# Optimization experiments

Hardware: AMD Instinct MI355X
Metric: run time of the kernel (lower is better)

The kernel has to match this reference:

```python
import jax, jax.numpy as jnp
import numpy as np

# dims
P = 16            # patch size
IMG = 224
D = 768           # embed dim
DEPTH = 12
DI = 1536         # d_inner = expand * D
N = 16            # d_state
DCONV = 4
DTR = 48          # dt_rank = ceil(D / 16)
GS = IMG // P     # 14
L = GS * GS       # 196
KEEP = 49         # (1 - 0.75) * 196
EPS = 1e-5


def _pos2d(embed_dim, gs):
    # replicates get_2d_sincos_pos_embed (numpy, fp32)
    def emb1(ed, pos):
        omega = np.arange(ed // 2, dtype=np.float32) / (ed / 2.0)
        omega = 1.0 / 10000 ** omega
        out = np.einsum('m,d->md', pos.reshape(-1).astype(np.float32), omega)
        return np.concatenate([np.sin(out), np.cos(out)], axis=1)
    gh = np.arange(gs, dtype=np.float32)
    grid = np.meshgrid(gh, gh)  # (w, h) per source
    return np.concatenate([emb1(embed_dim // 2, grid[0]), emb1(embed_dim // 2, grid[1])], axis=1)


def _ln(x, w, b):
    mu = x.mean(-1, keepdims=True)
    var = ((x - mu) ** 2).mean(-1, keepdims=True)
    return (x - mu) * jax.lax.rsqrt(var + EPS) * w + b


def setup_inputs() -> dict:
    key = jax.random.key(0)
    ks = jax.random.split(key, 12)
    s = 0.02
    dt = jnp.exp(jax.random.uniform(ks[7], (DEPTH, DI)) * (np.log(0.1) - np.log(0.001)) + np.log(0.001))
    return {
        'imgs': jax.random.normal(ks[0], (8, 3, IMG, IMG), jnp.float32),
        'noise': jax.random.uniform(ks[1], (8, L), jnp.float32),
        'patch_w': s * jax.random.normal(ks[2], (D, 3, P, P), jnp.float32),
        'patch_b': jnp.zeros((D,), jnp.float32),
        'pos_embed': jnp.asarray(_pos2d(D, GS), jnp.float32),            # [L, D]
        'ln_w': jnp.ones((DEPTH, D), jnp.float32),
        'ln_b': jnp.zeros((DEPTH, D), jnp.float32),
        'in_proj_w': s * jax.random.normal(ks[3], (DEPTH, 2 * DI, D), jnp.float32),
        'conv_w': 0.1 * jax.random.normal(ks[4], (DEPTH, DI, 1, DCONV), jnp.float32),
        'conv_b': jnp.zeros((DEPTH, DI), jnp.float32),
        'x_proj_w': s * jax.random.normal(ks[5], (DEPTH, DTR + 2 * N, DI), jnp.float32),
        'dt_w': s * jax.random.normal(ks[6], (DEPTH, DI, DTR), jnp.float32),
        'dt_b': jnp.log(jnp.expm1(dt)),                                   # inverse softplus
        'A_log': jnp.broadcast_to(jnp.log(jnp.arange(1, N + 1, dtype=jnp.float32)), (DEPTH, DI, N)).copy(),
        'D_skip': jnp.ones((DEPTH, DI), jnp.float32),
        'ssm_ln_w': jnp.ones((DEPTH, DI), jnp.float32),
        'ssm_ln_b': jnp.zeros((DEPTH, DI), jnp.float32),
        'out_proj_w': s * jax.random.normal(ks[8], (DEPTH, D, DI), jnp.float32),
        'final_ln_w': jnp.ones((D,), jnp.float32),
        'final_ln_b': jnp.zeros((D,), jnp.float32),
    }


def _encoder(imgs, noise, patch_w, patch_b, pos_embed, ln_w, ln_b, in_proj_w, conv_w,
             conv_b, x_proj_w, dt_w, dt_b, A_log, D_skip, ssm_ln_w, ssm_ln_b,
             out_proj_w, final_ln_w, final_ln_b):
    B = imgs.shape[0]
    # patch embed: conv stride=kernel=P -> [B, D, 14, 14] -> [B, L, D]
    x = jax.lax.conv_general_dilated(imgs, patch_w, (P, P), 'VALID',
                                     dimension_numbers=('NCHW', 'OIHW', 'NCHW'))
    x = (x + patch_b[None, :, None, None]).reshape(B, D, L).transpose(0, 2, 1)
    x = x + pos_embed[None]

    # random masking (MAE): keep KEEP tokens per sample
    ids_shuffle = jnp.argsort(noise, axis=1)
    ids_restore = jnp.argsort(ids_shuffle, axis=1)
    ids_keep = ids_shuffle[:, :KEEP]
    x = jnp.take_along_axis(x, ids_keep[:, :, None], axis=1)  # [B, KEEP, D]
    mask = jnp.ones((B, L), jnp.float32).at[:, :KEEP].set(0.0)
    mask = jnp.take_along_axis(mask, ids_restore, axis=1)

    def block_step(carry, lp):
        hs, res = carry
        lnw, lnb, ipw, cw, cb, xpw, dtw, dtb, alog, dsk, slw, slb, opw = lp
        res = res + hs                       # Add
        h = _ln(res, lnw, lnb)               # LN
        # --- Mamba mixer ---
        xz = h @ ipw.T                       # [B,K,2*DI]
        xi, z = jnp.split(xz, 2, axis=-1)
        xc = xi.transpose(0, 2, 1)           # [B,DI,K]
        xc = jnp.pad(xc, ((0, 0), (0, 0), (DCONV - 1, 0)))  # causal depthwise conv
        xc = jax.lax.conv_general_dilated(xc, cw, (1,), 'VALID',
                                          dimension_numbers=('NCH', 'OIH', 'NCH'),
                                          feature_group_count=DI)
        xc = jax.nn.silu(xc + cb[None, :, None]).transpose(0, 2, 1)  # [B,K,DI]
        xdbl = xc @ xpw.T                    # [B,K,DTR+2N]
        dtr, Bm, Cm = jnp.split(xdbl, [DTR, DTR + N], axis=-1)
        dt = jax.nn.softplus(dtr @ dtw.T + dtb)      # [B,K,DI]
        A = -jnp.exp(alog)                            # [DI,N]
        dA = jnp.exp(dt[..., None] * A)               # [B,K,DI,N]
        dBx = (dt * xc)[..., None] * Bm[:, :, None, :]
        def scan_step(hstate, inp):
            dA_t, dBx_t, C_t = inp
            hstate = dA_t * hstate + dBx_t            # [B,DI,N]
            y = jnp.einsum('bdn,bn->bd', hstate, C_t)
            return hstate, y
        h0 = jnp.zeros((xc.shape[0], DI, N), xc.dtype)
        _, ys = jax.lax.scan(scan_step, h0,
                             (dA.transpose(1, 0, 2, 3), dBx.transpose(1, 0, 2, 3), Cm.transpose(1, 0, 2)))
        y = ys.transpose(1, 0, 2) + dsk * xc          # D skip
        y = _ln(y, slw, slb)                           # norm after SSM
        y = y * jax.nn.silu(z)                         # gate
        out = y @ opw.T                                # [B,K,D]
        return (out, res), None

    res0 = jnp.zeros_like(x)
    (hs, res), _ = jax.lax.scan(block_step, (x, res0),
                                (ln_w, ln_b, in_proj_w, conv_w, conv_b, x_proj_w, dt_w,
                                 dt_b, A_log, D_skip, ssm_ln_w, ssm_ln_b, out_proj_w))
    latent = _ln(res + hs, final_ln_w, final_ln_b)
    return latent, mask, ids_restore


def reference(imgs, noise, patch_w, patch_b, pos_embed, ln_w, ln_b, in_proj_w, conv_w,
              conv_b, x_proj_w, dt_w, dt_b, A_log, D_skip, ssm_ln_w, ssm_ln_b,
              out_proj_w, final_ln_w, final_ln_b):
    return _encoder(imgs, noise, patch_w, patch_b, pos_embed, ln_w, ln_b, in_proj_w,
                    conv_w, conv_b, x_proj_w, dt_w, dt_b, A_log, D_skip, ssm_ln_w,
                    ssm_ln_b, out_proj_w, final_ln_w, final_ln_b)
```

## Files before the change

kernel.cpp:

```cpp
#include <hip/hip_runtime.h>
#include <cstdint>
#include <cstddef>

namespace {

constexpr int kD    = 768;
constexpr int kDI   = 1536;
constexpr int kN    = 16;
constexpr int kDTR  = 48;
constexpr int kL    = 196;
constexpr int kKeep = 49;
constexpr int kB    = 8;
constexpr int kTok  = kB * kKeep;
constexpr int kPatchRows = kB * kL;
constexpr float kEps = 1e-5f;

typedef __attribute__((ext_vector_type(8))) short short8;
typedef __attribute__((ext_vector_type(4))) float f32x4;

__device__ __forceinline__ short f2bf(float f) {
  unsigned u = __float_as_uint(f);
  return (short)((u + 0x7FFFu + ((u >> 16) & 1u)) >> 16);
}

__device__ __forceinline__ short8 pack8(float4 a, float4 b) {
  short8 r;
  r[0] = f2bf(a.x); r[1] = f2bf(a.y); r[2] = f2bf(a.z); r[3] = f2bf(a.w);
  r[4] = f2bf(b.x); r[5] = f2bf(b.y); r[6] = f2bf(b.z); r[7] = f2bf(b.w);
  return r;
}

__device__ __forceinline__ float silu(float x) { return x / (1.f + expf(-x)); }

__device__ __forceinline__ float block_sum256(float x, float* sbuf) {
#pragma unroll
  for (int o = 32; o > 0; o >>= 1) x += __shfl_down(x, o, 64);
  int wid = threadIdx.x >> 6;
  if ((threadIdx.x & 63) == 0) sbuf[wid] = x;
  __syncthreads();
  float r = sbuf[0] + sbuf[1] + sbuf[2] + sbuf[3];
  __syncthreads();
  return r;
}

__global__ __launch_bounds__(256) void im2col_kernel(const float* __restrict__ imgs,
                                                     float* __restrict__ A2) {
  int idx = blockIdx.x * 256 + threadIdx.x;
  if (idx >= kPatchRows * kD) return;
  int col = idx % kD;
  int row = idx / kD;
  int b = row / kL, l = row % kL;
  int gy = l / 14, gx = l % 14;
  int c   = col >> 8;
  int rem = col & 255;
  int py = rem >> 4, px = rem & 15;
  A2[idx] = imgs[((b * 3 + c) * 224 + gy * 16 + py) * 224 + gx * 16 + px];
}

template <int SPLIT, int ACT, bool KG>
__global__ __launch_bounds__(256) void gemm_mfma(const float* __restrict__ A, int lda,
                                                 const float* __restrict__ W,
                                                 const float* __restrict__ bias,
                                                 float* __restrict__ C, int ldc,
                                                 int M, int N, int K) {
  __shared__ __align__(16) short As[8][64][8];
  __shared__ __align__(16) short Bs[8][64][8];
  const int tid = threadIdx.x;
  const int bm = blockIdx.x * 64;
  const int bn = blockIdx.y * 64;
  const int kc = K / SPLIT;
  const int k0 = blockIdx.z * kc;
  const int nk = (kc + 63) / 64;
  const int sr = tid >> 2;
  const int sq = tid & 3;
  const int lane = tid & 63;
  const int wm = ((tid >> 6) >> 1) * 32;
  const int wn = ((tid >> 6) & 1) * 32;
  const bool mok = (bm + sr) < M;
  const bool nok = (bn + sr) < N;
  const float* Ap = A + (size_t)(bm + sr) * lda + k0 + sq * 16;
  const float* Wp = W + (size_t)(bn + sr) * K + k0 + sq * 16;

  f32x4 acc[2][2];
#pragma unroll
  for (int i = 0; i < 2; ++i)
#pragma unroll
    for (int j = 0; j < 2; ++j) acc[i][j] = (f32x4){0.f, 0.f, 0.f, 0.f};

  for (int kt = 0; kt < nk; ++kt) {
    const int kb = kt * 64;
    const float4 z4 = make_float4(0.f, 0.f, 0.f, 0.f);
    float4 a0 = z4, a1 = z4, a2 = z4, a3 = z4;
    float4 w0 = z4, w1 = z4, w2 = z4, w3 = z4;
    const float* ap = Ap + kb;
    const float* wp = Wp + kb;
    if (!KG) {
      if (mok) {
        a0 = *(const float4*)ap;       a1 = *(const float4*)(ap + 4);
        a2 = *(const float4*)(ap + 8); a3 = *(const float4*)(ap + 12);
      }
      if (nok) {
        w0 = *(const float4*)wp;       w1 = *(const float4*)(wp + 4);
        w2 = *(const float4*)(wp + 8); w3 = *(const float4*)(wp + 12);
      }
    } else {
      const int kq = k0 + kb + sq * 16;
      if (mok) {
        if (kq + 4  <= K) a0 = *(const float4*)ap;
        if (kq + 8  <= K) a1 = *(const float4*)(ap + 4);
        if (kq + 12 <= K) a2 = *(const float4*)(ap + 8);
        if (kq + 16 <= K) a3 = *(const float4*)(ap + 12);
      }
      if (nok) {
        if (kq + 4  <= K) w0 = *(const float4*)wp;
        if (kq + 8  <= K) w1 = *(const float4*)(wp + 4);
        if (kq + 12 <= K) w2 = *(const float4*)(wp + 8);
        if (kq + 16 <= K) w3 = *(const float4*)(wp + 12);
      }
    }
    if (kt) __syncthreads();
    *(short8*)&As[sq * 2][sr][0]     = pack8(a0, a1);
    *(short8*)&As[sq * 2 + 1][sr][0] = pack8(a2, a3);
    *(short8*)&Bs[sq * 2][sr][0]     = pack8(w0, w1);
    *(short8*)&Bs[sq * 2 + 1][sr][0] = pack8(w2, w3);
    __syncthreads();
#pragma unroll
    for (int kh = 0; kh < 2; ++kh) {
      const int kg = kh * 4 + (lane >> 4);
      short8 af0 = *(const short8*)&As[kg][wm + (lane & 15)][0];
      short8 af1 = *(const short8*)&As[kg][wm + 16 + (lane & 15)][0];
      short8 bf0 = *(const short8*)&Bs[kg][wn + (lane & 15)][0];
      short8 bf1 = *(const short8*)&Bs[kg][wn + 16 + (lane & 15)][0];
      acc[0][0] = __builtin_amdgcn_mfma_f32_16x16x32_bf16(af0, bf0, acc[0][0], 0, 0, 0);
      acc[0][1] = __builtin_amdgcn_mfma_f32_16x16x32_bf16(af0, bf1, acc[0][1], 0, 0, 0);
      acc[1][0] = __builtin_amdgcn_mfma_f32_16x16x32_bf16(af1, bf0, acc[1][0], 0, 0, 0);
      acc[1][1] = __builtin_amdgcn_mfma_f32_16x16x32_bf16(af1, bf1, acc[1][1], 0, 0, 0);
    }
  }

  const int mrow = (lane >> 4) * 4;
  const int ncol = lane & 15;
#pragma unroll
  for (int i2 = 0; i2 < 2; ++i2)
#pragma unroll
    for (int j2 = 0; j2 < 2; ++j2) {
      int n = bn + wn + j2 * 16 + ncol;
      if (n >= N) continue;
      float bv = (SPLIT == 1 && bias) ? bias[n] : 0.f;
#pragma unroll
      for (int r = 0; r < 4; ++r) {
        int m = bm + wm + i2 * 16 + mrow + r;
        if (m >= M) continue;
        float v = acc[i2][j2][r];
        if (SPLIT == 1) {
          v += bv;
          if (ACT == 1) v = (v > 20.f) ? v : log1pf(expf(v));
          C[(size_t)m * ldc + n] = v;
        } else {
          C[(size_t)blockIdx.z * ((size_t)M * N) + (size_t)m * N + n] = v;
        }
      }
    }
}

__global__ __launch_bounds__(256) void gemm_xdbl_conv(const float* __restrict__ xz,
                                                      const float* __restrict__ cw,
                                                      const float* __restrict__ cb,
                                                      const float* __restrict__ W,
                                                      float* __restrict__ Cpart) {
  __shared__ __align__(16) short As[8][64][8];
  __shared__ __align__(16) short Bs[8][64][8];
  const int tid = threadIdx.x;
  const int bm = blockIdx.x * 64;
  const int bn = blockIdx.y * 64;
  const int k0 = blockIdx.z * 64;
  const int sr = tid >> 2;
  const int sq = tid & 3;
  const int lane = tid & 63;
  const int wm = ((tid >> 6) >> 1) * 32;
  const int wn = ((tid >> 6) & 1) * 32;
  const int m = bm + sr;
  const bool mok = m < kTok;
  const bool nok = (bn + sr) < 80;
  const float4 z4 = make_float4(0.f, 0.f, 0.f, 0.f);

  float4 a[4] = {z4, z4, z4, z4};
  if (mok) {
    const int b = m / kKeep, t = m % kKeep;
    const int dbase = k0 + sq * 16;
#pragma unroll
    for (int g = 0; g < 4; ++g) {
      const int d = dbase + g * 4;
      float4 cacc = *(const float4*)&cb[d];
      float4 c0 = *(const float4*)&cw[(d + 0) * 4];
      float4 c1 = *(const float4*)&cw[(d + 1) * 4];
      float4 c2 = *(const float4*)&cw[(d + 2) * 4];
      float4 c3 = *(const float4*)&cw[(d + 3) * 4];
      const float t0[4] = {c0.x, c0.y, c0.z, c0.w};
      const float t1[4] = {c1.x, c1.y, c1.z, c1.w};
      const float t2[4] = {c2.x, c2.y, c2.z, c2.w};
      const float t3[4] = {c3.x, c3.y, c3.z, c3.w};
#pragma unroll
      for (int j = 0; j < 4; ++j) {
        int tt = t - 3 + j;
        if (tt < 0) continue;
        float4 xv = *(const float4*)&xz[(size_t)(b * kKeep + tt) * 3072 + d];
        cacc.x += xv.x * t0[j];
        cacc.y += xv.y * t1[j];
        cacc.z += xv.z * t2[j];
        cacc.w += xv.w * t3[j];
      }
      cacc.x = silu(cacc.x); cacc.y = silu(cacc.y);
      cacc.z = silu(cacc.z); cacc.w = silu(cacc.w);
      a[g] = cacc;
    }
  }
  float4 w0 = z4, w1 = z4, w2 = z4, w3 = z4;
  if (nok) {
    const float* wp = W + (size_t)(bn + sr) * kDI + k0 + sq * 16;
    w0 = *(const float4*)wp;       w1 = *(const float4*)(wp + 4);
    w2 = *(const float4*)(wp + 8); w3 = *(const float4*)(wp + 12);
  }
  *(short8*)&As[sq * 2][sr][0]     = pack8(a[0], a[1]);
  *(short8*)&As[sq * 2 + 1][sr][0] = pack8(a[2], a[3]);
  *(short8*)&Bs[sq * 2][sr][0]     = pack8(w0, w1);
  *(short8*)&Bs[sq * 2 + 1][sr][0] = pack8(w2, w3);
  __syncthreads();

  f32x4 acc[2][2];
#pragma unroll
  for (int i = 0; i < 2; ++i)
#pragma unroll
    for (int j = 0; j < 2; ++j) acc[i][j] = (f32x4){0.f, 0.f, 0.f, 0.f};
#pragma unroll
  for (int kh = 0; kh < 2; ++kh) {
    const int kg = kh * 4 + (lane >> 4);
    short8 af0 = *(const short8*)&As[kg][wm + (lane & 15)][0];
    short8 af1 = *(const short8*)&As[kg][wm + 16 + (lane & 15)][0];
    short8 bf0 = *(const short8*)&Bs[kg][wn + (lane & 15)][0];
    short8 bf1 = *(const short8*)&Bs[kg][wn + 16 + (lane & 15)][0];
    acc[0][0] = __builtin_amdgcn_mfma_f32_16x16x32_bf16(af0, bf0, acc[0][0], 0, 0, 0);
    acc[0][1] = __builtin_amdgcn_mfma_f32_16x16x32_bf16(af0, bf1, acc[0][1], 0, 0, 0);
    acc[1][0] = __builtin_amdgcn_mfma_f32_16x16x32_bf16(af1, bf0, acc[1][0], 0, 0, 0);
    acc[1][1] = __builtin_amdgcn_mfma_f32_16x16x32_bf16(af1, bf1, acc[1][1], 0, 0, 0);
  }

  const int mrow = (lane >> 4) * 4;
  const int ncol = lane & 15;
#pragma unroll
  for (int i2 = 0; i2 < 2; ++i2)
#pragma unroll
    for (int j2 = 0; j2 < 2; ++j2) {
      int n = bn + wn + j2 * 16 + ncol;
      if (n >= 80) continue;
#pragma unroll
      for (int r = 0; r < 4; ++r) {
        int mm = bm + wm + i2 * 16 + mrow + r;
        if (mm >= kTok) continue;
        Cpart[(size_t)blockIdx.z * (kTok * 80) + (size_t)mm * 80 + n] =
            acc[i2][j2][r];
      }
    }
}

__global__ __launch_bounds__(256) void reduce_kernel(const float* __restrict__ part,
                                                     float* __restrict__ out,
                                                     int total4, int Z) {
  int i = blockIdx.x * 256 + threadIdx.x;
  if (i >= total4) return;
  const float4* p = (const float4*)part;
  float4 s = p[i];
  for (int z = 1; z < Z; ++z) {
    float4 v = p[(size_t)z * total4 + i];
    s.x += v.x; s.y += v.y; s.z += v.z; s.w += v.w;
  }
  ((float4*)out)[i] = s;
}

__global__ __launch_bounds__(256) void sort_kernel(const float* __restrict__ noise,
                                                   int* __restrict__ ids_keep,
                                                   float* __restrict__ mask_out,
                                                   float* __restrict__ idsr_out) {
  __shared__ float nb[kL];
  int b = blockIdx.x;
  int t = threadIdx.x;
  if (t < kL) nb[t] = noise[b * kL + t];
  __syncthreads();
  if (t < kL) {
    float v = nb[t];
    int rank = 0;
    for (int j = 0; j < kL; ++j) {
      float u = nb[j];
      rank += (u < v || (u == v && j < t)) ? 1 : 0;
    }
    if (rank < kKeep) ids_keep[b * kKeep + rank] = t;
    idsr_out[b * kL + t] = (float)rank;
    mask_out[b * kL + t] = (rank < kKeep) ? 0.f : 1.f;
  }
}

__global__ __launch_bounds__(256) void gather_kernel(const float* __restrict__ x0,
                                                     const int* __restrict__ ids_keep,
                                                     const float* __restrict__ pos,
                                                     float* __restrict__ hs) {
  int m = blockIdx.x;
  int b = m / kKeep, k = m % kKeep;
  int l = ids_keep[b * kKeep + k];
  const float* src = x0 + (size_t)(b * kL + l) * kD;
  const float* pp  = pos + (size_t)l * kD;
  float* dst = hs + (size_t)m * kD;
  for (int d = threadIdx.x; d < kD; d += 256) dst[d] = src[d] + pp[d];
}

template <int DD, int NP>
__global__ __launch_bounds__(256) void add_ln_kernel(const float* __restrict__ part,
                                                     float* __restrict__ res,
                                                     const float* __restrict__ w,
                                                     const float* __restrict__ b,
                                                     float* __restrict__ out) {
  constexpr int PT = DD / 256;
  __shared__ float sbuf[4];
  int m = blockIdx.x;
  int t = threadIdx.x;
  float v[PT];
  float s = 0.f;
#pragma unroll
  for (int i = 0; i < PT; ++i) {
    int d = t + i * 256;
    float acc = res[(size_t)m * DD + d];
#pragma unroll
    for (int z = 0; z < NP; ++z)
      acc += part[(size_t)z * (kTok * DD) + (size_t)m * DD + d];
    v[i] = acc;
    s += acc;
  }
  float mean = block_sum256(s, sbuf) * (1.f / DD);
  float s2 = 0.f;
#pragma unroll
  for (int i = 0; i < PT; ++i) { float d0 = v[i] - mean; s2 += d0 * d0; }
  float var = block_sum256(s2, sbuf) * (1.f / DD);
  float rstd = rsqrtf(var + kEps);
#pragma unroll
  for (int i = 0; i < PT; ++i) {
    int d = t + i * 256;
    res[(size_t)m * DD + d] = v[i];
    out[(size_t)m * DD + d] = (v[i] - mean) * rstd * w[d] + b[d];
  }
}

__global__ __launch_bounds__(256) void scan_state_kernel(
    const float* __restrict__ dt,
    const float* __restrict__ xz,
    const float* __restrict__ xdbl,
    const float* __restrict__ cw, const float* __restrict__ cb,
    const float* __restrict__ A_log, const float* __restrict__ D_skip,
    float* __restrict__ y) {
  __shared__ float dts[kKeep][16];
  __shared__ float xzs[kKeep][16];
  __shared__ float bcs[kKeep][32];
  __shared__ float ys[kKeep][16];
  const int d0 = blockIdx.x * 16;
  const int b  = blockIdx.y;
  const int tid = threadIdx.x;
  for (int i = tid; i < kKeep * 16; i += 256) {
    int t = i >> 4, c = i & 15;
    dts[t][c] = dt[(size_t)(b * kKeep + t) * kDI + d0 + c];
    xzs[t][c] = xz[(size_t)(b * kKeep + t) * 3072 + d0 + c];
  }
  for (int i = tid; i < kKeep * 32; i += 256) {
    int t = i >> 5, c = i & 31;
    bcs[t][c] = xdbl[(size_t)(b * kKeep + t) * 80 + kDTR + c];
  }
  __syncthreads();

  const int ch = tid >> 4;
  const int n  = tid & 15;
  const int d  = d0 + ch;
  const float Aval = -expf(A_log[(size_t)d * kN + n]);
  const float dsk  = D_skip[d];
  const float4 cw4 = *(const float4*)&cw[d * 4];
  const float cb0  = cb[d];

  float s = 0.f;
  float w0 = 0.f, w1 = 0.f, w2 = 0.f;
  for (int t = 0; t < kKeep; ++t) {
    float xin = xzs[t][ch];
    float cacc = cb0 + w0 * cw4.x + w1 * cw4.y + w2 * cw4.z + xin * cw4.w;
    w0 = w1; w1 = w2; w2 = xin;
    float xcv = silu(cacc);
    float dtv = dts[t][ch];
    s = expf(dtv * Aval) * s + (dtv * xcv) * bcs[t][n];
    float yp = s * bcs[t][16 + n];
    yp += __shfl_xor(yp, 1, 64);
    yp += __shfl_xor(yp, 2, 64);
    yp += __shfl_xor(yp, 4, 64);
    yp += __shfl_xor(yp, 8, 64);
    if (n == 0) ys[t][ch] = yp + dsk * xcv;
  }
  __syncthreads();
  for (int i = tid; i < kKeep * 16; i += 256)
    y[(size_t)(b * kKeep + (i >> 4)) * kDI + d0 + (i & 15)] = ys[i >> 4][i & 15];
}

__global__ __launch_bounds__(256) void ssm_ln_silu_kernel(const float* __restrict__ y,
                                                          const float* __restrict__ xz,
                                                          const float* __restrict__ w,
                                                          const float* __restrict__ b,
                                                          float* __restrict__ y2) {
  constexpr int PT = kDI / 256;
  __shared__ float sbuf[4];
  int m = blockIdx.x;
  int t = threadIdx.x;
  float v[PT];
  float s = 0.f;
#pragma unroll
  for (int i = 0; i < PT; ++i) {
    int d = t + i * 256;
    v[i] = y[(size_t)m * kDI + d];
    s += v[i];
  }
  float mean = block_sum256(s, sbuf) * (1.f / kDI);
  float s2 = 0.f;
#pragma unroll
  for (int i = 0; i < PT; ++i) { float d0 = v[i] - mean; s2 += d0 * d0; }
  float var = block_sum256(s2, sbuf) * (1.f / kDI);
  float rstd = rsqrtf(var + kEps);
#pragma unroll
  for (int i = 0; i < PT; ++i) {
    int d = t + i * 256;
    float z = xz[(size_t)m * 3072 + kDI + d];
    y2[(size_t)m * kDI + d] =
        ((v[i] - mean) * rstd * w[d] + b[d]) * silu(z);
  }
}

}

extern "C" void kernel_launch(void* const* d_in, const int* in_sizes, int n_in,
                              void* d_out, int out_size, void* d_ws, size_t ws_size,
                              hipStream_t stream) {
  const float* imgs       = (const float*)d_in[0];
  const float* noise      = (const float*)d_in[1];
  const float* patch_w    = (const float*)d_in[2];
  const float* patch_b    = (const float*)d_in[3];
  const float* pos_embed  = (const float*)d_in[4];
  const float* ln_w       = (const float*)d_in[5];
  const float* ln_b       = (const float*)d_in[6];
  const float* in_proj_w  = (const float*)d_in[7];
  const float* conv_w     = (const float*)d_in[8];
  const float* conv_b     = (const float*)d_in[9];
  const float* x_proj_w   = (const float*)d_in[10];
  const float* dt_w       = (const float*)d_in[11];
  const float* dt_b       = (const float*)d_in[12];
  const float* A_log      = (const float*)d_in[13];
  const float* D_skip     = (const float*)d_in[14];
  const float* ssm_ln_w   = (const float*)d_in[15];
  const float* ssm_ln_b   = (const float*)d_in[16];
  const float* out_proj_w = (const float*)d_in[17];
  const float* final_ln_w = (const float*)d_in[18];
  const float* final_ln_b = (const float*)d_in[19];

  float* out      = (float*)d_out;
  float* latent   = out;
  float* mask_out = out + 301056;
  float* idsr_out = out + 301056 + 1568;

  float* ws        = (float*)d_ws;
  float* hs        = ws;
  float* res       = hs + 301056;
  float* h         = res + 301056;
  float* xz        = h + 301056;
  float* xdbl      = xz + 1204224;
  float* dtb_      = xdbl + 31360;
  float* part_xdbl = dtb_ + 602112;
  float* part_out  = part_xdbl + 752640;
  float* ybuf      = part_out + 1204224;
  float* y2        = ybuf + 602112;
  int*   ids_keep  = (int*)(y2 + 602112);
  float* A2 = xz;
  float* x0 = part_xdbl;

  {
    int tot = kPatchRows * kD;
    im2col_kernel<<<(tot + 255) / 256, 256, 0, stream>>>(imgs, A2);
    gemm_mfma<1, 0, false><<<dim3(25, 12, 1), 256, 0, stream>>>(
        A2, kD, patch_w, patch_b, x0, kD, kPatchRows, kD, kD);
  }

  sort_kernel<<<kB, 256, 0, stream>>>(noise, ids_keep, mask_out, idsr_out);

  gather_kernel<<<kTok, 256, 0, stream>>>(x0, ids_keep, pos_embed, hs);

  hipMemsetAsync(res, 0, (size_t)kTok * kD * sizeof(float), stream);

  for (int l = 0; l < 12; ++l) {
    const float* lnw  = ln_w  + (size_t)l * kD;
    const float* lnb  = ln_b  + (size_t)l * kD;
    const float* ipw  = in_proj_w  + (size_t)l * 2 * kDI * kD;
    const float* cw   = conv_w     + (size_t)l * kDI * 4;
    const float* cb   = conv_b     + (size_t)l * kDI;
    const float* xpw  = x_proj_w   + (size_t)l * (kDTR + 2 * kN) * kDI;
    const float* dtw  = dt_w       + (size_t)l * kDI * kDTR;
    const float* dtbv = dt_b       + (size_t)l * kDI;
    const float* alog = A_log      + (size_t)l * kDI * kN;
    const float* dsk  = D_skip     + (size_t)l * kDI;
    const float* slw  = ssm_ln_w   + (size_t)l * kDI;
    const float* slb  = ssm_ln_b   + (size_t)l * kDI;
    const float* opw  = out_proj_w + (size_t)l * kD * kDI;

    if (l == 0)
      add_ln_kernel<kD, 1><<<kTok, 256, 0, stream>>>(hs, res, lnw, lnb, h);
    else
      add_ln_kernel<kD, 4><<<kTok, 256, 0, stream>>>(part_out, res, lnw, lnb, h);

    gemm_mfma<1, 0, false><<<dim3(7, 48, 1), 256, 0, stream>>>(
        h, kD, ipw, nullptr, xz, 2 * kDI, kTok, 2 * kDI, kD);

    gemm_xdbl_conv<<<dim3(7, 2, 24), 256, 0, stream>>>(xz, cw, cb, xpw, part_xdbl);
    reduce_kernel<<<(7840 + 255) / 256, 256, 0, stream>>>(part_xdbl, xdbl, 7840, 24);

    gemm_mfma<1, 1, true><<<dim3(7, 24, 1), 256, 0, stream>>>(
        xdbl, 80, dtw, dtbv, dtb_, kDI, kTok, kDI, kDTR);

    scan_state_kernel<<<dim3(96, kB), 256, 0, stream>>>(dtb_, xz, xdbl, cw, cb,
                                                        alog, dsk, ybuf);

    ssm_ln_silu_kernel<<<kTok, 256, 0, stream>>>(ybuf, xz, slw, slb, y2);

    gemm_mfma<4, 0, false><<<dim3(7, 12, 4), 256, 0, stream>>>(
        y2, kDI, opw, nullptr, part_out, kD, kTok, kD, kDI);
  }

  add_ln_kernel<kD, 4><<<kTok, 256, 0, stream>>>(part_out, res, final_ln_w,
                                                 final_ln_b, latent);
}
```

Measured before the change: 1.379 ms.

## Fuse dt projection and softplus into scan kernel; double-buffer GEMM LDS tiles

The separate dt_proj GEMM launch (K=48) is removed. The scan kernel now loads the dt-rank slice of xdbl and the matching dt_w rows into shared memory and computes dt plus softplus per channel itself. This saves one launch per layer and the write and read of the dt buffer. The generic GEMM also gains double-buffered shared-memory tiles, prefetching the next K tile into registers while the MFMAs run, which removes one barrier per iteration. In exchange the GEMM uses twice the LDS, which may lower occupancy, and the scan kernel does extra per-block dot-product work.

```diff
diff --git a/kernel.cpp b/kernel.cpp
--- a/kernel.cpp
+++ b/kernel.cpp
@@ -57,20 +57,20 @@
   A2[idx] = imgs[((b * 3 + c) * 224 + gy * 16 + py) * 224 + gx * 16 + px];
 }
 
-template <int SPLIT, int ACT, bool KG>
+template <int SPLIT>
 __global__ __launch_bounds__(256) void gemm_mfma(const float* __restrict__ A, int lda,
                                                  const float* __restrict__ W,
                                                  const float* __restrict__ bias,
                                                  float* __restrict__ C, int ldc,
                                                  int M, int N, int K) {
-  __shared__ __align__(16) short As[8][64][8];
-  __shared__ __align__(16) short Bs[8][64][8];
+  __shared__ __align__(16) short As[2][8][64][8];
+  __shared__ __align__(16) short Bs[2][8][64][8];
   const int tid = threadIdx.x;
   const int bm = blockIdx.x * 64;
   const int bn = blockIdx.y * 64;
   const int kc = K / SPLIT;
   const int k0 = blockIdx.z * kc;
-  const int nk = (kc + 63) / 64;
+  const int nk = kc / 64;
   const int sr = tid >> 2;
   const int sq = tid & 3;
   const int lane = tid & 63;
@@ -80,61 +80,68 @@
   const bool nok = (bn + sr) < N;
   const float* Ap = A + (size_t)(bm + sr) * lda + k0 + sq * 16;
   const float* Wp = W + (size_t)(bn + sr) * K + k0 + sq * 16;
-
-  f32x4 acc[2][2];
-#pragma unroll
-  for (int i = 0; i < 2; ++i)
-#pragma unroll
-    for (int j = 0; j < 2; ++j) acc[i][j] = (f32x4){0.f, 0.f, 0.f, 0.f};
-
-  for (int kt = 0; kt < nk; ++kt) {
-    const int kb = kt * 64;
-    const float4 z4 = make_float4(0.f, 0.f, 0.f, 0.f);
+  const float4 z4 = make_float4(0.f, 0.f, 0.f, 0.f);
+
+  {
     float4 a0 = z4, a1 = z4, a2 = z4, a3 = z4;
     float4 w0 = z4, w1 = z4, w2 = z4, w3 = z4;
-    const float* ap = Ap + kb;
-    const float* wp = Wp + kb;
-    if (!KG) {
+    if (mok) {
+      a0 = *(const float4*)Ap;       a1 = *(const float4*)(Ap + 4);
+      a2 = *(const float4*)(Ap + 8); a3 = *(const float4*)(Ap + 12);
+    }
+    if (nok) {
+      w0 = *(const float4*)Wp;       w1 = *(const float4*)(Wp + 4);
+      w2 = *(const float4*)(Wp + 8); w3 = *(const float4*)(Wp + 12);
+    }
+    *(short8*)&As[0][sq * 2][sr][0]     = pack8(a0, a1);
+    *(short8*)&As[0][sq * 2 + 1][sr][0] = pack8(a2, a3);
+    *(short8*)&Bs[0][sq * 2][sr][0]     = pack8(w0, w1);
+    *(short8*)&Bs[0][sq * 2 + 1][sr][0] = pack8(w2, w3);
+  }
+  __syncthreads();
+
+  f32x4 acc[2][2];
+#pragma unroll
+  for (int i = 0; i < 2; ++i)
+#pragma unroll
+    for (int j = 0; j < 2; ++j) acc[i][j] = (f32x4){0.f, 0.f, 0.f, 0.f};
+
+  for (int kt = 0; kt < nk; ++kt) {
+    const int cur = kt & 1;
+    float4 na0 = z4, na1 = z4, na2 = z4, na3 = z4;
+    float4 nw0 = z4, nw1 = z4, nw2 = z4, nw3 = z4;
+    const bool more = (kt + 1) < nk;
+    if (more) {
+      const float* ap = Ap + (kt + 1) * 64;
+      const float* wp = Wp + (kt + 1) * 64;
       if (mok) {
-        a0 = *(const float4*)ap;       a1 = *(const float4*)(ap + 4);
-        a2 = *(const float4*)(ap + 8); a3 = *(const float4*)(ap + 12);
+        na0 = *(const float4*)ap;       na1 = *(const float4*)(ap + 4);
+        na2 = *(const float4*)(ap + 8); na3 = *(const float4*)(ap + 12);
       }
       if (nok) {
-        w0 = *(const float4*)wp;       w1 = *(const float4*)(wp + 4);
-        w2 = *(const float4*)(wp + 8); w3 = *(const float4*)(wp + 12);
+        nw0 = *(const float4*)wp;       nw1 = *(const float4*)(wp + 4);
+        nw2 = *(const float4*)(wp + 8); nw3 = *(const float4*)(wp + 12);
       }
-    } else {
-      const int kq = k0 + kb + sq * 16;
-      if (mok) {
-        if (kq + 4  <= K) a0 = *(const float4*)ap;
-        if (kq + 8  <= K) a1 = *(const float4*)(ap + 4);
-        if (kq + 12 <= K) a2 = *(const float4*)(ap + 8);
-        if (kq + 16 <= K) a3 = *(const float4*)(ap + 12);
-      }
-      if (nok) {
-        if (kq + 4  <= K) w0 = *(const float4*)wp;
-        if (kq + 8  <= K) w1 = *(const float4*)(wp + 4);
-        if (kq + 12 <= K) w2 = *(const float4*)(wp + 8);
-        if (kq + 16 <= K) w3 = *(const float4*)(wp + 12);
-      }
-    }
-    if (kt) __syncthreads();
-    *(short8*)&As[sq * 2][sr][0]     = pack8(a0, a1);
-    *(short8*)&As[sq * 2 + 1][sr][0] = pack8(a2, a3);
-    *(short8*)&Bs[sq * 2][sr][0]     = pack8(w0, w1);
-    *(short8*)&Bs[sq * 2 + 1][sr][0] = pack8(w2, w3);
-    __syncthreads();
+    }
 #pragma unroll
     for (int kh = 0; kh < 2; ++kh) {
       const int kg = kh * 4 + (lane >> 4);
-      short8 af0 = *(const short8*)&As[kg][wm + (lane & 15)][0];
-      short8 af1 = *(const short8*)&As[kg][wm + 16 + (lane & 15)][0];
-      short8 bf0 = *(const short8*)&Bs[kg][wn + (lane & 15)][0];
-      short8 bf1 = *(const short8*)&Bs[kg][wn + 16 + (lane & 15)][0];
+      short8 af0 = *(const short8*)&As[cur][kg][wm + (lane & 15)][0];
+      short8 af1 = *(const short8*)&As[cur][kg][wm + 16 + (lane & 15)][0];
+      short8 bf0 = *(const short8*)&Bs[cur][kg][wn + (lane & 15)][0];
+      short8 bf1 = *(const short8*)&Bs[cur][kg][wn + 16 + (lane & 15)][0];
       acc[0][0] = __builtin_amdgcn_mfma_f32_16x16x32_bf16(af0, bf0, acc[0][0], 0, 0, 0);
       acc[0][1] = __builtin_amdgcn_mfma_f32_16x16x32_bf16(af0, bf1, acc[0][1], 0, 0, 0);
       acc[1][0] = __builtin_amdgcn_mfma_f32_16x16x32_bf16(af1, bf0, acc[1][0], 0, 0, 0);
       acc[1][1] = __builtin_amdgcn_mfma_f32_16x16x32_bf16(af1, bf1, acc[1][1], 0, 0, 0);
+    }
+    if (more) {
+      const int nxt = cur ^ 1;
+      *(short8*)&As[nxt][sq * 2][sr][0]     = pack8(na0, na1);
+      *(short8*)&As[nxt][sq * 2 + 1][sr][0] = pack8(na2, na3);
+      *(short8*)&Bs[nxt][sq * 2][sr][0]     = pack8(nw0, nw1);
+      *(short8*)&Bs[nxt][sq * 2 + 1][sr][0] = pack8(nw2, nw3);
+      __syncthreads();
     }
   }
 
@@ -153,9 +160,7 @@
         if (m >= M) continue;
         float v = acc[i2][j2][r];
         if (SPLIT == 1) {
-          v += bv;
-          if (ACT == 1) v = (v > 20.f) ? v : log1pf(expf(v));
-          C[(size_t)m * ldc + n] = v;
+          C[(size_t)m * ldc + n] = v + bv;
         } else {
           C[(size_t)blockIdx.z * ((size_t)M * N) + (size_t)m * N + n] = v;
         }
@@ -349,27 +354,53 @@
 }
 
 __global__ __launch_bounds__(256) void scan_state_kernel(
-    const float* __restrict__ dt,
     const float* __restrict__ xz,
     const float* __restrict__ xdbl,
     const float* __restrict__ cw, const float* __restrict__ cb,
+    const float* __restrict__ dtw,
+    const float* __restrict__ dtbv,
     const float* __restrict__ A_log, const float* __restrict__ D_skip,
     float* __restrict__ y) {
+  __shared__ __align__(16) float dtr_s[kKeep][kDTR];
+  __shared__ __align__(16) float dtw_s[16][52];
+  __shared__ float bcs[kKeep][32];
   __shared__ float dts[kKeep][16];
   __shared__ float xzs[kKeep][16];
-  __shared__ float bcs[kKeep][32];
   __shared__ float ys[kKeep][16];
   const int d0 = blockIdx.x * 16;
   const int b  = blockIdx.y;
   const int tid = threadIdx.x;
+  for (int i = tid; i < kKeep * 80; i += 256) {
+    int t = i / 80, c = i % 80;
+    float v = xdbl[(size_t)(b * kKeep + t) * 80 + c];
+    if (c < kDTR) dtr_s[t][c] = v;
+    else bcs[t][c - kDTR] = v;
+  }
   for (int i = tid; i < kKeep * 16; i += 256) {
     int t = i >> 4, c = i & 15;
-    dts[t][c] = dt[(size_t)(b * kKeep + t) * kDI + d0 + c];
     xzs[t][c] = xz[(size_t)(b * kKeep + t) * 3072 + d0 + c];
   }
-  for (int i = tid; i < kKeep * 32; i += 256) {
-    int t = i >> 5, c = i & 31;
-    bcs[t][c] = xdbl[(size_t)(b * kKeep + t) * 80 + kDTR + c];
+  for (int i = tid; i < 16 * kDTR; i += 256)
+    dtw_s[i / kDTR][i % kDTR] = dtw[(size_t)(d0 + i / kDTR) * kDTR + i % kDTR];
+  __syncthreads();
+
+  {
+    const int c = tid & 15;
+    const int tg = tid >> 4;
+    float4 wreg[12];
+#pragma unroll
+    for (int q = 0; q < 12; ++q) wreg[q] = *(const float4*)&dtw_s[c][q * 4];
+    const float dtb0 = dtbv[d0 + c];
+    for (int t = tg; t < kKeep; t += 16) {
+      float acc = dtb0;
+#pragma unroll
+      for (int q = 0; q < 12; ++q) {
+        float4 r = *(const float4*)&dtr_s[t][q * 4];
+        acc += r.x * wreg[q].x + r.y * wreg[q].y +
+               r.z * wreg[q].z + r.w * wreg[q].w;
+      }
+      dts[t][c] = (acc > 20.f) ? acc : log1pf(expf(acc));
+    }
   }
   __syncthreads();
 
@@ -471,8 +502,7 @@
   float* h         = res + 301056;
   float* xz        = h + 301056;
   float* xdbl      = xz + 1204224;
-  float* dtb_      = xdbl + 31360;
-  float* part_xdbl = dtb_ + 602112;
+  float* part_xdbl = xdbl + 31360;
   float* part_out  = part_xdbl + 752640;
   float* ybuf      = part_out + 1204224;
   float* y2        = ybuf + 602112;
@@ -483,7 +513,7 @@
   {
     int tot = kPatchRows * kD;
     im2col_kernel<<<(tot + 255) / 256, 256, 0, stream>>>(imgs, A2);
-    gemm_mfma<1, 0, false><<<dim3(25, 12, 1), 256, 0, stream>>>(
+    gemm_mfma<1><<<dim3(25, 12, 1), 256, 0, stream>>>(
         A2, kD, patch_w, patch_b, x0, kD, kPatchRows, kD, kD);
   }
 
@@ -513,21 +543,18 @@
     else
       add_ln_kernel<kD, 4><<<kTok, 256, 0, stream>>>(part_out, res, lnw, lnb, h);
 
-    gemm_mfma<1, 0, false><<<dim3(7, 48, 1), 256, 0, stream>>>(
+    gemm_mfma<1><<<dim3(7, 48, 1), 256, 0, stream>>>(
         h, kD, ipw, nullptr, xz, 2 * kDI, kTok, 2 * kDI, kD);
 
     gemm_xdbl_conv<<<dim3(7, 2, 24), 256, 0, stream>>>(xz, cw, cb, xpw, part_xdbl);
     reduce_kernel<<<(7840 + 255) / 256, 256, 0, stream>>>(part_xdbl, xdbl, 7840, 24);
 
-    gemm_mfma<1, 1, true><<<dim3(7, 24, 1), 256, 0, stream>>>(
-        xdbl, 80, dtw, dtbv, dtb_, kDI, kTok, kDI, kDTR);
-
-    scan_state_kernel<<<dim3(96, kB), 256, 0, stream>>>(dtb_, xz, xdbl, cw, cb,
-                                                        alog, dsk, ybuf);
+    scan_state_kernel<<<dim3(96, kB), 256, 0, stream>>>(xz, xdbl, cw, cb, dtw,
+                                                        dtbv, alog, dsk, ybuf);
 
     ssm_ln_silu_kernel<<<kTok, 256, 0, stream>>>(ybuf, xz, slw, slb, y2);
 
-    gemm_mfma<4, 0, false><<<dim3(7, 12, 4), 256, 0, stream>>>(
+    gemm_mfma<4><<<dim3(7, 12, 4), 256, 0, stream>>>(
         y2, kDI, opw, nullptr, part_out, kD, kTok, kD, kDI);
   }
 
```

After: 1.350 ms. 1.02x faster.
